# Optimization experiments

Measured on AMD Instinct MI355X. Metric: run time of the kernel, lower is better.

The kernel has to match this reference:

```python
import jax, jax.numpy as jnp
import numpy as np

GAMMA = 1.0


def setup_inputs() -> dict:
    key = jax.random.key(0)
    kx, ky = jax.random.split(key)
    x = jax.random.normal(kx, (8192, 128), dtype=jnp.float32)
    y = jax.random.normal(ky, (8192, 128), dtype=jnp.float32)
    return {"x": x, "y": y}


def reference(x, y):
    # RBF kernel K[i,j] = exp(-gamma * ||x_i - y_j||^2)
    x2 = jnp.sum(x * x, axis=1)              # [N]
    y2 = jnp.sum(y * y, axis=1)              # [M]
    xy = jnp.einsum('nd,md->nm', x, y)       # [N, M] GEMM
    sq = x2[:, None] + y2[None, :] - 2.0 * xy
    sq = jnp.maximum(sq, 0.0)                # guard tiny negatives from cancellation
    return jnp.exp(-GAMMA * sq)
```

## Files before the change

kernel.cpp:

```cpp
#include <hip/hip_runtime.h>
#include <hip/hip_bf16.h>

typedef __bf16 bf16x8 __attribute__((ext_vector_type(8)));
typedef float f32x4 __attribute__((ext_vector_type(4)));
typedef unsigned short us4 __attribute__((ext_vector_type(4)));

__device__ __forceinline__ unsigned short f2bf(float f) {
    unsigned u = __float_as_uint(f);
    u += 0x7fffu + ((u >> 16) & 1u);
    return (unsigned short)(u >> 16);
}

__global__ __launch_bounds__(256)
void rbf_prep(const float* __restrict__ X, const float* __restrict__ Y,
              unsigned short* __restrict__ Xb, unsigned short* __restrict__ Yb,
              float* __restrict__ x2, float* __restrict__ y2) {
    const int b = blockIdx.x;
    const float* src = (b < 128) ? X : Y;
    unsigned short* db = (b < 128) ? Xb : Yb;
    float* dn = (b < 128) ? x2 : y2;
    const int r0 = (b & 127) * 64;
    const int t = threadIdx.x;
    const f32x4* s4 = (const f32x4*)(src + (size_t)r0 * 128);
#pragma unroll
    for (int i = 0; i < 8; ++i) {
        int idx = i * 256 + t;
        int r = idx >> 5, c4 = idx & 31;
        f32x4 v = s4[idx];
        us4 o;
        o.x = f2bf(v[0]); o.y = f2bf(v[1]); o.z = f2bf(v[2]); o.w = f2bf(v[3]);
        int pc = (c4 >> 1) ^ (r & 7);
        *(us4*)&db[(size_t)(r0 + r) * 128 + pc * 8 + (c4 & 1) * 4] = o;
    }
    if (t < 64) {
        const f32x4* row = (const f32x4*)(src + (size_t)(r0 + t) * 128);
        float s = 0.f;
#pragma unroll
        for (int c = 0; c < 32; ++c) {
            f32x4 v = row[c];
            s += v[0] * v[0] + v[1] * v[1] + v[2] * v[2] + v[3] * v[3];
        }
        dn[r0 + t] = s;
    }
}

__global__ __launch_bounds__(256, 3)
void rbf_main(const unsigned short* __restrict__ Xb, const unsigned short* __restrict__ Yb,
              const float* __restrict__ x2, const float* __restrict__ y2,
              float* __restrict__ O, int ldo) {
    __shared__ __align__(16) char smem[49152];
    unsigned short* Ab = (unsigned short*)smem;
    unsigned short* Bb = (unsigned short*)(smem + 16384);
    float*          Ol = (float*)smem;

    const int t = threadIdx.x, l = t & 63, w = t >> 6;
    const int col0 = blockIdx.x * 128, row0 = blockIdx.y * 64;

    const char* gA = (const char*)(Xb + (size_t)row0 * 128);
    const char* gB = (const char*)(Yb + (size_t)col0 * 128);
#pragma unroll
    for (int j = 0; j < 4; ++j) {
        int base = (w * 4 + j) * 1024;
        __builtin_amdgcn_global_load_lds(
            (const __attribute__((address_space(1))) void*)(gA + base + l * 16),
            (__attribute__((address_space(3))) void*)(smem + base), 16, 0, 0);
    }
#pragma unroll
    for (int j = 0; j < 8; ++j) {
        int base = (w * 8 + j) * 1024;
        __builtin_amdgcn_global_load_lds(
            (const __attribute__((address_space(1))) void*)(gB + base + l * 16),
            (__attribute__((address_space(3))) void*)(smem + 16384 + base), 16, 0, 0);
    }

    const int lr = l & 15, q = l >> 4;
    const int wr = (w >> 1) * 32, wc = (w & 1) * 64;

    f32x4 x2v[2]; float y2v[4];
#pragma unroll
    for (int m = 0; m < 2; ++m) x2v[m] = *(const f32x4*)&x2[row0 + wr + m * 16 + q * 4];
#pragma unroll
    for (int n = 0; n < 4; ++n) y2v[n] = y2[col0 + wc + n * 16 + lr];

    __syncthreads();

    f32x4 acc[2][4] = {};
#pragma unroll
    for (int k = 0; k < 4; ++k) {
        bf16x8 af[2], bv[4];
#pragma unroll
        for (int m = 0; m < 2; ++m) {
            int R = wr + m * 16 + lr;
            af[m] = *(const bf16x8*)((const char*)Ab + R * 256 + (((k << 2) + q) ^ (R & 7)) * 16);
        }
#pragma unroll
        for (int n = 0; n < 4; ++n) {
            int R = wc + n * 16 + lr;
            bv[n] = *(const bf16x8*)((const char*)Bb + R * 256 + (((k << 2) + q) ^ (R & 7)) * 16);
        }
#pragma unroll
        for (int m = 0; m < 2; ++m)
#pragma unroll
            for (int n = 0; n < 4; ++n)
                acc[m][n] = __builtin_amdgcn_mfma_f32_16x16x32_bf16(af[m], bv[n], acc[m][n], 0, 0, 0);
    }

    __syncthreads();

#pragma unroll
    for (int m = 0; m < 2; ++m) {
        int rloc = wr + m * 16 + q * 4;
#pragma unroll
        for (int n = 0; n < 4; ++n) {
            int col = wc + n * 16 + lr;
            int lc = col >> 2;
            float yv = y2v[n];
#pragma unroll
            for (int i = 0; i < 4; ++i) {
                int row = rloc + i;
                float sq = fmaxf(x2v[m][i] + yv - 2.0f * acc[m][n][i], 0.f);
                int pc = (lc & 24) | ((lc ^ row) & 7);
                Ol[row * 128 + pc * 4 + (col & 3)] = __expf(-sq);
            }
        }
    }
    __syncthreads();

#pragma unroll
    for (int i = 0; i < 8; ++i) {
        int idx = i * 256 + t;
        int r = idx >> 5, lcc = idx & 31;
        int pc = (lcc & 24) | ((lcc ^ r) & 7);
        f32x4 v = *(const f32x4*)((const char*)Ol + r * 512 + pc * 16);
        *(float4*)&O[(size_t)(row0 + r) * ldo + col0 + lcc * 4] = *(float4*)&v;
    }
}

extern "C" void kernel_launch(void* const* d_in, const int* in_sizes, int n_in,
                              void* d_out, int out_size, void* d_ws, size_t ws_size,
                              hipStream_t stream) {
    const float* X = (const float*)d_in[0];
    const float* Y = (const float*)d_in[1];
    float* O = (float*)d_out;
    const int N = in_sizes[0] / 128;
    const int M = in_sizes[1] / 128;
    unsigned short* Xb = (unsigned short*)d_ws;
    unsigned short* Yb = Xb + (size_t)N * 128;
    float* x2 = (float*)(Yb + (size_t)M * 128);
    float* y2 = x2 + N;
    rbf_prep<<<dim3((N + M) / 64), 256, 0, stream>>>(X, Y, Xb, Yb, x2, y2);
    rbf_main<<<dim3(M / 128, N / 64), 256, 0, stream>>>(Xb, Yb, x2, y2, O, M);
}
```

Measured before the change: 277.3 us.

## Shrink main tile to 64x64, per-wave epilogue staging, fold log2e into norms

The main kernel tile shrinks from 64x128 to 64x64, cutting LDS from 48KB to 32KB and raising the launch-bounds occupancy hint from 3 to 5 blocks. The output staging becomes per-wave, which removes a block-wide barrier before the stores. The squared norms are prescaled by -log2(e) in the prep kernel so the epilogue is one fma, a min and exp2f instead of scaling plus __expf. The smaller tile halves operand reuse and doubles the block count, and the leading dimension is now hardcoded to 8192.

```diff
diff --git a/kernel.cpp b/kernel.cpp
--- a/kernel.cpp
+++ b/kernel.cpp
@@ -4,6 +4,8 @@
 typedef __bf16 bf16x8 __attribute__((ext_vector_type(8)));
 typedef float f32x4 __attribute__((ext_vector_type(4)));
 typedef unsigned short us4 __attribute__((ext_vector_type(4)));
+
+#define NLOG2E -1.44269504088896340736f
 
 __device__ __forceinline__ unsigned short f2bf(float f) {
     unsigned u = __float_as_uint(f);
@@ -14,11 +16,11 @@
 __global__ __launch_bounds__(256)
 void rbf_prep(const float* __restrict__ X, const float* __restrict__ Y,
               unsigned short* __restrict__ Xb, unsigned short* __restrict__ Yb,
-              float* __restrict__ x2, float* __restrict__ y2) {
+              float* __restrict__ x2n, float* __restrict__ y2n) {
     const int b = blockIdx.x;
     const float* src = (b < 128) ? X : Y;
     unsigned short* db = (b < 128) ? Xb : Yb;
-    float* dn = (b < 128) ? x2 : y2;
+    float* dn = (b < 128) ? x2n : y2n;
     const int r0 = (b & 127) * 64;
     const int t = threadIdx.x;
     const f32x4* s4 = (const f32x4*)(src + (size_t)r0 * 128);
@@ -40,21 +42,20 @@
             f32x4 v = row[c];
             s += v[0] * v[0] + v[1] * v[1] + v[2] * v[2] + v[3] * v[3];
         }
-        dn[r0 + t] = s;
+        dn[r0 + t] = NLOG2E * s;
     }
 }
 
-__global__ __launch_bounds__(256, 3)
+__global__ __launch_bounds__(256, 5)
 void rbf_main(const unsigned short* __restrict__ Xb, const unsigned short* __restrict__ Yb,
-              const float* __restrict__ x2, const float* __restrict__ y2,
-              float* __restrict__ O, int ldo) {
-    __shared__ __align__(16) char smem[49152];
+              const float* __restrict__ x2n, const float* __restrict__ y2n,
+              float* __restrict__ O) {
+    __shared__ __align__(16) char smem[32768];
     unsigned short* Ab = (unsigned short*)smem;
     unsigned short* Bb = (unsigned short*)(smem + 16384);
-    float*          Ol = (float*)smem;
 
     const int t = threadIdx.x, l = t & 63, w = t >> 6;
-    const int col0 = blockIdx.x * 128, row0 = blockIdx.y * 64;
+    const int col0 = blockIdx.x * 64, row0 = blockIdx.y * 64;
 
     const char* gA = (const char*)(Xb + (size_t)row0 * 128);
     const char* gB = (const char*)(Yb + (size_t)col0 * 128);
@@ -64,75 +65,71 @@
         __builtin_amdgcn_global_load_lds(
             (const __attribute__((address_space(1))) void*)(gA + base + l * 16),
             (__attribute__((address_space(3))) void*)(smem + base), 16, 0, 0);
-    }
-#pragma unroll
-    for (int j = 0; j < 8; ++j) {
-        int base = (w * 8 + j) * 1024;
         __builtin_amdgcn_global_load_lds(
             (const __attribute__((address_space(1))) void*)(gB + base + l * 16),
             (__attribute__((address_space(3))) void*)(smem + 16384 + base), 16, 0, 0);
     }
 
     const int lr = l & 15, q = l >> 4;
-    const int wr = (w >> 1) * 32, wc = (w & 1) * 64;
+    const int wr = (w >> 1) * 32, wc = (w & 1) * 32;
 
-    f32x4 x2v[2]; float y2v[4];
+    f32x4 xn[2]; float yn[2];
 #pragma unroll
-    for (int m = 0; m < 2; ++m) x2v[m] = *(const f32x4*)&x2[row0 + wr + m * 16 + q * 4];
+    for (int m = 0; m < 2; ++m) xn[m] = *(const f32x4*)&x2n[row0 + wr + m * 16 + q * 4];
 #pragma unroll
-    for (int n = 0; n < 4; ++n) y2v[n] = y2[col0 + wc + n * 16 + lr];
+    for (int n = 0; n < 2; ++n) yn[n] = y2n[col0 + wc + n * 16 + lr];
 
     __syncthreads();
 
-    f32x4 acc[2][4] = {};
+    f32x4 acc[2][2] = {};
 #pragma unroll
     for (int k = 0; k < 4; ++k) {
-        bf16x8 af[2], bv[4];
+        bf16x8 af[2], bv[2];
 #pragma unroll
         for (int m = 0; m < 2; ++m) {
             int R = wr + m * 16 + lr;
             af[m] = *(const bf16x8*)((const char*)Ab + R * 256 + (((k << 2) + q) ^ (R & 7)) * 16);
         }
 #pragma unroll
-        for (int n = 0; n < 4; ++n) {
+        for (int n = 0; n < 2; ++n) {
             int R = wc + n * 16 + lr;
             bv[n] = *(const bf16x8*)((const char*)Bb + R * 256 + (((k << 2) + q) ^ (R & 7)) * 16);
         }
 #pragma unroll
         for (int m = 0; m < 2; ++m)
 #pragma unroll
-            for (int n = 0; n < 4; ++n)
+            for (int n = 0; n < 2; ++n)
                 acc[m][n] = __builtin_amdgcn_mfma_f32_16x16x32_bf16(af[m], bv[n], acc[m][n], 0, 0, 0);
     }
 
     __syncthreads();
 
+    float* Ol = (float*)(smem + w * 4096);
 #pragma unroll
     for (int m = 0; m < 2; ++m) {
-        int rloc = wr + m * 16 + q * 4;
 #pragma unroll
-        for (int n = 0; n < 4; ++n) {
-            int col = wc + n * 16 + lr;
+        for (int n = 0; n < 2; ++n) {
+            int col = n * 16 + lr;
             int lc = col >> 2;
-            float yv = y2v[n];
+            float ynv = yn[n];
 #pragma unroll
             for (int i = 0; i < 4; ++i) {
-                int row = rloc + i;
-                float sq = fmaxf(x2v[m][i] + yv - 2.0f * acc[m][n][i], 0.f);
-                int pc = (lc & 24) | ((lc ^ row) & 7);
-                Ol[row * 128 + pc * 4 + (col & 3)] = __expf(-sq);
+                int row = m * 16 + q * 4 + i;
+                float arg = fmaf(-2.0f * NLOG2E, acc[m][n][i], xn[m][i] + ynv);
+                arg = fminf(arg, 0.f);
+                int pc = (lc ^ row) & 7;
+                Ol[row * 32 + pc * 4 + (col & 3)] = exp2f(arg);
             }
         }
     }
-    __syncthreads();
 
 #pragma unroll
-    for (int i = 0; i < 8; ++i) {
-        int idx = i * 256 + t;
-        int r = idx >> 5, lcc = idx & 31;
-        int pc = (lcc & 24) | ((lcc ^ r) & 7);
-        f32x4 v = *(const f32x4*)((const char*)Ol + r * 512 + pc * 16);
-        *(float4*)&O[(size_t)(row0 + r) * ldo + col0 + lcc * 4] = *(float4*)&v;
+    for (int it = 0; it < 4; ++it) {
+        int r = it * 8 + (l >> 3);
+        int lc2 = l & 7;
+        int pc = lc2 ^ (r & 7);
+        f32x4 v = *(const f32x4*)((const char*)Ol + r * 128 + pc * 16);
+        *(float4*)&O[(size_t)(row0 + wr + r) * 8192 + col0 + wc + lc2 * 4] = *(float4*)&v;
     }
 }
 
@@ -146,8 +143,8 @@
     const int M = in_sizes[1] / 128;
     unsigned short* Xb = (unsigned short*)d_ws;
     unsigned short* Yb = Xb + (size_t)N * 128;
-    float* x2 = (float*)(Yb + (size_t)M * 128);
-    float* y2 = x2 + N;
-    rbf_prep<<<dim3((N + M) / 64), 256, 0, stream>>>(X, Y, Xb, Yb, x2, y2);
-    rbf_main<<<dim3(M / 128, N / 64), 256, 0, stream>>>(Xb, Yb, x2, y2, O, M);
+    float* x2n = (float*)(Yb + (size_t)M * 128);
+    float* y2n = x2n + N;
+    rbf_prep<<<dim3((N + M) / 64), 256, 0, stream>>>(X, Y, Xb, Yb, x2n, y2n);
+    rbf_main<<<dim3(M / 64, N / 64), 256, 0, stream>>>(Xb, Yb, x2n, y2n, O);
 }
```

Result: slower. 285.2 us (+2.9%).
